# Optimization experiments

Hardware: AMD Instinct MI355X
Metric: run time of the kernel (lower is better)

The kernel has to match this reference:

```python
import jax, jax.numpy as jnp
import numpy as np

H = 5
THETA = 1e-4
RHO = 1e-5


def setup_inputs() -> dict:
    key = jax.random.key(0)
    kw, kb, kv = jax.random.split(key, 3)
    # keras random_normal_initializer(mean=0.5/0.1, stddev=0.05) + NonNeg constraint
    w = jnp.abs(0.5 + 0.05 * jax.random.normal(kw, (1, H), dtype=jnp.float32))
    b = jnp.abs(0.1 + 0.05 * jax.random.normal(kb, (H - 1,), dtype=jnp.float32))
    v = jnp.abs(0.5 + 0.05 * jax.random.normal(kv, (H, 1), dtype=jnp.float32))
    return {"w": w, "b": b, "v": v, "k": 16384}


def _gen_gaps(w, b, v, k):
    dt = jnp.float32
    wf = jnp.reshape(w, (-1,)).astype(dt)            # (H,)
    vf = jnp.reshape(v, (-1,)).astype(dt)            # (H,)
    bf = jnp.concatenate([jnp.zeros((1,), dt), b.astype(dt)])  # (H,), b[0]==0
    v0 = -jnp.dot(bf, vf)                            # scalar, matches -(b @ v)
    c = jnp.asarray(THETA + RHO, dt)
    p = jnp.asarray(THETA / (THETA + RHO), dt)
    K2 = k + 2

    def inverse(x):
        # faithful to source: only breakpoint i=0 is used (for i in range(1))
        b_over_w = -bf / wf
        r_x = jnp.dot(jax.nn.relu(wf * b_over_w[0] + bf), vf) + v0  # scalar
        bounds = jnp.sort(jnp.stack([jnp.asarray(0.0, dt), r_x, jnp.asarray(jnp.inf, dt)]))
        pos = jnp.searchsorted(bounds, x, side='right')
        # argsort of length-1 r_x is [0]; v_b/v_w are length-1 gathers
        v_b0 = vf[0] * bf[0]
        v_w0 = vf[0] * wf[0]
        gate = (pos >= 2).astype(dt)                 # sum over [:pos-1] of length-1 arrays
        num = x - v0 - gate * v_b0
        deo = gate * v_w0
        safe = jnp.where(deo != 0, deo, jnp.asarray(1.0, dt))
        return jnp.where(deo != 0, num / safe, jnp.asarray(0.0, dt))  # divide_no_nan

    key = jax.random.key(1234)
    key, k0 = jax.random.split(key)
    z0 = -jnp.log(jax.random.uniform(k0, (), dtype=dt))
    x0 = inverse(z0)

    max_steps = 2 * K2 + 256  # safe bound: ~1.1*(k+2) steps needed in expectation

    def step(carry, subkey):
        j, pos, x, inner = carry
        u1, u2, u3, u4 = jax.random.uniform(subkey, (4,), dtype=dt)
        active = j < K2
        do_inner = inner & active
        do_outer = jnp.logical_and(~inner, active)
        # --- outer body: u = runif(); z = rexp(); x = inverse(z + r(u*x)) ---
        u_x = u1 * x
        z = -jnp.log(u2)
        r_u_x = v0 + jnp.dot(jax.nn.relu(wf * u_x + bf), vf)
        x_new = inverse(z + r_u_x)
        x2 = jnp.where(do_outer, x_new, x)
        # --- inner write (inner mode records pos BEFORE the increment) ---
        wgate = do_inner.astype(dt)
        val = pos * wgate
        idx = jnp.where(do_inner, j, K2)  # dummy slot K2 when not writing
        j2 = j + do_inner.astype(j.dtype)
        # --- pos += rexp() / (x * (theta + rho)) in both modes ---
        e = -jnp.log(u3)
        pos2 = pos + jnp.where(active, e / (x2 * c), jnp.asarray(0.0, dt))
        # --- inner-loop continuation check: runif() < theta/(theta+rho) and j < k+2 ---
        inner2 = jnp.where(active, (u4 < p) & (j2 < K2), inner)
        return (j2, pos2, x2, inner2), (val, idx)

    keys = jax.random.split(key, max_steps)
    init = (jnp.int32(0), jnp.asarray(0.0, dt), x0, jnp.asarray(False))
    _, (vals, idxs) = jax.lax.scan(step, init, keys)
    ta = jnp.zeros((K2 + 1,), dt).at[idxs].add(vals)[:K2]  # TensorArray of size k+2
    ret = ta[1:]
    diff = ret[1:] - ret[:-1]
    return diff.reshape(1, k)


def reference(w, b, v, k):
    return _gen_gaps(w, b, v, k)
```

## Files before the change

kernel.cpp:

```cpp
#include <hip/hip_runtime.h>
#include <stdint.h>

#define H_MAX 8
#define NT 4096
#define K1T 256
#define K1B (NT / K1T)
#define K2T 1024
#define NW 16

__host__ __device__ __forceinline__ uint32_t rotl32(uint32_t v, int d) {
  return (v << d) | (v >> (32 - d));
}

__host__ __device__ __forceinline__ void tf2x32(uint32_t k0, uint32_t k1,
                                                uint32_t x0, uint32_t x1,
                                                uint32_t& o0, uint32_t& o1) {
  const uint32_t ks2 = k0 ^ k1 ^ 0x1BD11BDAu;
#define TFR(d) { x0 += x1; x1 = rotl32(x1, d); x1 ^= x0; }
  x0 += k0; x1 += k1;
  TFR(13) TFR(15) TFR(26) TFR(6)
  x0 += k1;  x1 += ks2 + 1u;
  TFR(17) TFR(29) TFR(16) TFR(24)
  x0 += ks2; x1 += k0 + 2u;
  TFR(13) TFR(15) TFR(26) TFR(6)
  x0 += k0;  x1 += k1 + 3u;
  TFR(17) TFR(29) TFR(16) TFR(24)
  x0 += k1;  x1 += ks2 + 4u;
  TFR(13) TFR(15) TFR(26) TFR(6)
  x0 += ks2; x1 += k0 + 5u;
#undef TFR
  o0 = x0; o1 = x1;
}

__device__ __forceinline__ float u01f(uint32_t bits) {
  return __uint_as_float((bits >> 9) | 0x3f800000u) - 1.0f;
}

__device__ __forceinline__ uint32_t pbits32(uint32_t k0, uint32_t k1, uint32_t i) {
  uint32_t o0, o1;
  tf2x32(k0, k1, 0u, i, o0, o1);
  return o0 ^ o1;
}

__global__ __launch_bounds__(K1T) void rng_kernel(const float* __restrict__ w,
                                                  const float* __restrict__ bb,
                                                  const float* __restrict__ vv,
                                                  float4* __restrict__ pre,
                                                  float* __restrict__ out,
                                                  int k, int H,
                                                  uint32_t sk0, uint32_t sk1) {
  const int t = blockIdx.x * K1T + threadIdx.x;

  float wf[H_MAX], bf[H_MAX], vf[H_MAX];
  for (int h = 0; h < H; ++h) {
    wf[h] = w[h];
    vf[h] = vv[h];
    bf[h] = (h == 0) ? 0.0f : bb[h - 1];
  }
  float sbv = 0.0f, swv = 0.0f;
  for (int h = 0; h < H; ++h) { sbv += bf[h] * vf[h]; swv += wf[h] * vf[h]; }
  const float ivw  = 1.0f / (vf[0] * wf[0]);
  const float GAIN = swv * ivw;
  const float C_F  = (float)(0.0001 + 1e-05);
  const float RCF  = 1.0f / C_F;

  for (int i4 = t; i4 * 4 + 3 < k; i4 += NT)
    ((float4*)out)[i4] = make_float4(0.0f, 0.0f, 0.0f, 0.0f);

  uint32_t a0, a1;
  tf2x32(sk0, sk1, 0u, (uint32_t)t, a0, a1);
  float u1 = u01f(pbits32(a0, a1, 0u));
  float Z  = -logf(u01f(pbits32(a0, a1, 1u)));
  float E  = -logf(u01f(pbits32(a0, a1, 2u)));
  float u4 = u01f(pbits32(a0, a1, 3u));
  int slot = (t & 3) * K2T + (t >> 2);
  pre[slot] = make_float4(u1 * GAIN, (Z + sbv) * ivw, E * RCF, u4);
}

__global__ __launch_bounds__(K2T, 1) void scan_kernel(const float* __restrict__ w,
                                                      const float* __restrict__ bb,
                                                      const float* __restrict__ vv,
                                                      const float4* __restrict__ pre,
                                                      float* __restrict__ out,
                                                      int k, int K2, int B, int H,
                                                      uint32_t sk0, uint32_t sk1,
                                                      uint32_t z0bits) {
  __shared__ double Aw[NW], Cw[NW];
  __shared__ float  Sw[NW];
  __shared__ int    Fw[NW];
  __shared__ float  sh_u4[K2T];
  __shared__ float  ta[NT];
  __shared__ double finX;
  __shared__ float  finP;
  __shared__ int    jfin;

  const int tid  = threadIdx.x;
  const int lane = tid & 63;
  const int wid  = tid >> 6;

  float wf[H_MAX], bf[H_MAX], vf[H_MAX];
  for (int h = 0; h < H; ++h) {
    wf[h] = w[h];
    vf[h] = vv[h];
    bf[h] = (h == 0) ? 0.0f : bb[h - 1];
  }
  float sbv = 0.0f, swv = 0.0f;
  for (int h = 0; h < H; ++h) { sbv += bf[h] * vf[h]; swv += wf[h] * vf[h]; }
  const float ivw  = 1.0f / (vf[0] * wf[0]);
  const float GAIN = swv * ivw;
  const float C_F  = (float)(0.0001 + 1e-05);
  const float P_F  = (float)(0.0001 / (0.0001 + 1e-05));
  const float RCF  = 1.0f / C_F;
  const float INF  = __builtin_inff();

  float4 r0 = pre[0 * K2T + tid];
  float4 r1 = pre[1 * K2T + tid];
  float4 r2 = pre[2 * K2T + tid];
  float4 r3 = pre[3 * K2T + tid];

  sh_u4[tid] = r3.w;
  __syncthreads();
  float u4m1 = (tid == 0) ? 2.0f : sh_u4[tid - 1];
  bool fl0 = (u4m1 < P_F);
  bool fl1 = (r0.w < P_F);
  bool fl2 = (r1.w < P_F);
  bool fl3 = (r2.w < P_F);
  double a0d = fl0 ? 1.0 : (double)r0.x, c0d = fl0 ? 0.0 : (double)r0.y;
  double a1d = fl1 ? 1.0 : (double)r1.x, c1d = fl1 ? 0.0 : (double)r1.y;
  double a2d = fl2 ? 1.0 : (double)r2.x, c2d = fl2 ? 0.0 : (double)r2.y;
  double a3d = fl3 ? 1.0 : (double)r3.x, c3d = fl3 ? 0.0 : (double)r3.y;

  double A = 1.0, C = 0.0;
  C = a0d * C + c0d;  A = a0d * A;
  C = a1d * C + c1d;  A = a1d * A;
  C = a2d * C + c2d;  A = a2d * A;
  C = a3d * C + c3d;  A = a3d * A;
  for (int d = 1; d < 64; d <<= 1) {
    double Ap = __shfl_up(A, d);
    double Cp = __shfl_up(C, d);
    if (lane >= d) { C = A * Cp + C; A = A * Ap; }
  }
  if (lane == 63) { Aw[wid] = A; Cw[wid] = C; }
  __syncthreads();
  double Awp = 1.0, Cwp = 0.0;
  for (int q = 0; q < wid; ++q) {
    double Aq = Aw[q], Cq = Cw[q];
    Cwp = Aq * Cwp + Cq;
    Awp = Aq * Awp;
  }
  double Aex = __shfl_up(A, 1), Cex = __shfl_up(C, 1);
  if (lane == 0) { Aex = 1.0; Cex = 0.0; }
  double Ag = Aex * Awp;
  double Cg = Aex * Cwp + Cex;

  float z0  = -logf(u01f(z0bits));
  float x0f = (z0 + sbv) * ivw;
  double X = Ag * (double)x0f + Cg;
  float inc0, inc1, inc2, inc3;
  X = a0d * X + c0d;  inc0 = r0.z * __builtin_amdgcn_rcpf((float)X);
  X = a1d * X + c1d;  inc1 = r1.z * __builtin_amdgcn_rcpf((float)X);
  X = a2d * X + c2d;  inc2 = r2.z * __builtin_amdgcn_rcpf((float)X);
  X = a3d * X + c3d;  inc3 = r3.z * __builtin_amdgcn_rcpf((float)X);
  float Sl = inc0 + inc1 + inc2 + inc3;
  int Fl = (fl0 ? 1 : 0) + (fl1 ? 1 : 0) + (fl2 ? 1 : 0) + (fl3 ? 1 : 0);

  float S = Sl; int F = Fl;
  for (int d = 1; d < 64; d <<= 1) {
    float Sp = __shfl_up(S, d);
    int   Fp = __shfl_up(F, d);
    if (lane >= d) { S += Sp; F += Fp; }
  }
  if (lane == 63) { Sw[wid] = S; Fw[wid] = F; }
  __syncthreads();
  float Swp = 0.0f; int Fwp = 0;
  for (int q = 0; q < wid; ++q) { Swp += Sw[q]; Fwp += Fw[q]; }
  float Sex = __shfl_up(S, 1); int Fex = __shfl_up(F, 1);
  if (lane == 0) { Sex = 0.0f; Fex = 0; }
  float P0 = Swp + Sex;
  int   J0 = Fwp + Fex;

  {
    float P = P0; int J = J0;
    if (fl0) { if (J < NT) ta[J] = P; ++J; }  P += inc0;
    if (fl1) { if (J < NT) ta[J] = P; ++J; }  P += inc1;
    if (fl2) { if (J < NT) ta[J] = P; ++J; }  P += inc2;
    if (fl3) { if (J < NT) ta[J] = P; ++J; }  P += inc3;
    if (tid == K2T - 1) { finX = X; finP = P; jfin = J; }
  }
  __syncthreads();

  {
    int J = J0;
    if (fl0) { if (J >= 2 && J < NT && (J - 2) < k) out[J - 2] = ta[J] - ta[J - 1]; ++J; }
    if (fl1) { if (J >= 2 && J < NT && (J - 2) < k) out[J - 2] = ta[J] - ta[J - 1]; ++J; }
    if (fl2) { if (J >= 2 && J < NT && (J - 2) < k) out[J - 2] = ta[J] - ta[J - 1]; ++J; }
    if (fl3) { if (J >= 2 && J < NT && (J - 2) < k) out[J - 2] = ta[J] - ta[J - 1]; ++J; }
  }

  double Xf = finX;
  if (Xf >= 1e30) return;
  if (tid >= 64) return;
  {
    float x = (float)Xf;
    float rcx = __builtin_amdgcn_rcpf(x);
    float pos = finP;
    int j = jfin;
    float pos_prev = (j >= 1 && j <= NT) ? ta[j - 1] : 0.0f;
    bool inner = (sh_u4[K2T - 1] < P_F) && (j < K2);
    bool done = false;
    for (int base = NT; base < B && !done; base += 64) {
      int t = base + lane;
      if (t >= B) t = B - 1;
      uint32_t a0, a1;
      tf2x32(sk0, sk1, 0u, (uint32_t)t, a0, a1);
      float aa = u01f(pbits32(a0, a1, 0u)) * GAIN;
      float cc = (-logf(u01f(pbits32(a0, a1, 1u))) + sbv) * ivw;
      float EE = -logf(u01f(pbits32(a0, a1, 2u))) * RCF;
      float u4 = u01f(pbits32(a0, a1, 3u));
      int lim = (B - base) < 64 ? (B - base) : 64;
      for (int s = 0; s < lim; ++s) {
        float Af = __shfl(aa, s);
        float Cf = __shfl(cc, s);
        float Ef = __shfl(EE, s);
        float U4 = __shfl(u4, s);
        if (inner) {
          if (j >= 2 && (j - 2) < k) out[j - 2] = pos - pos_prev;
          pos_prev = pos; ++j;
        } else {
          x = __builtin_fmaf(Af, x, Cf);
          rcx = __builtin_amdgcn_rcpf(x);
        }
        pos = __builtin_fmaf(Ef, rcx, pos);
        inner = (U4 < P_F) && (j < K2);
        if (x == INF || j >= K2) {
          if (x == INF && j >= 2 && (j - 2) < k) out[j - 2] = pos - pos_prev;
          done = true; break;
        }
      }
    }
    if (!done && j >= 2 && (j - 2) < k) out[j - 2] = 0.0f - pos_prev;
  }
}

extern "C" void kernel_launch(void* const* d_in, const int* in_sizes, int n_in,
                              void* d_out, int out_size, void* d_ws, size_t ws_size,
                              hipStream_t stream) {
  const float* w = (const float*)d_in[0];
  const float* b = (const float*)d_in[1];
  const float* v = (const float*)d_in[2];
  (void)n_in; (void)ws_size;
  const int H  = in_sizes[0];
  const int k  = out_size;
  const int K2 = k + 2;
  const int B  = 2 * K2 + 256;

  uint32_t ka0, ka1, kb0, kb1;
  tf2x32(0u, 1234u, 0u, 0u, ka0, ka1);
  tf2x32(0u, 1234u, 0u, 1u, kb0, kb1);
  uint32_t zb0, zb1;
  tf2x32(kb0, kb1, 0u, 0u, zb0, zb1);
  const uint32_t z0bits = zb0 ^ zb1;

  float4* pre = (float4*)d_ws;

  rng_kernel<<<dim3(K1B), K1T, 0, stream>>>(w, b, v, pre, (float*)d_out,
                                            k, H, ka0, ka1);
  scan_kernel<<<dim3(1), K2T, 0, stream>>>(w, b, v, pre, (float*)d_out,
                                           k, K2, B, H, ka0, ka1, z0bits);
}
```

Baseline: 17.74 us.

## Fuse RNG and scan kernels into one launch with inter-block flag sync

Merges the RNG precompute kernel and the single-block scan kernel into one launch. Block 0 runs the scan and spin-waits on per-block flags in global memory, while 16 producer blocks each generate 256 RNG tuples, zero the output and set a magic flag after a threadfence. The goal is to remove the second kernel launch and the gap between launches. It relies on all 17 blocks being co-resident, adds spin-wait cost, and requires the flags to be reset to zero for the next call, which the scan block does.

```diff
diff --git a/kernel.cpp b/kernel.cpp
--- a/kernel.cpp
+++ b/kernel.cpp
@@ -3,10 +3,11 @@
 
 #define H_MAX 8
 #define NT 4096
-#define K1T 256
-#define K1B (NT / K1T)
 #define K2T 1024
 #define NW 16
+#define NRB 16
+#define RSTEPS 256
+#define MAGIC 0x5EED5EEDu
 
 __host__ __device__ __forceinline__ uint32_t rotl32(uint32_t v, int d) {
   return (v << d) | (v >> (32 - d));
@@ -42,14 +43,16 @@
   return o0 ^ o1;
 }
 
-__global__ __launch_bounds__(K1T) void rng_kernel(const float* __restrict__ w,
-                                                  const float* __restrict__ bb,
-                                                  const float* __restrict__ vv,
-                                                  float4* __restrict__ pre,
-                                                  float* __restrict__ out,
-                                                  int k, int H,
-                                                  uint32_t sk0, uint32_t sk1) {
-  const int t = blockIdx.x * K1T + threadIdx.x;
+__global__ __launch_bounds__(K2T, 1) void gaps_fused(const float* __restrict__ w,
+                                                     const float* __restrict__ bb,
+                                                     const float* __restrict__ vv,
+                                                     float4* __restrict__ pre,
+                                                     uint32_t* __restrict__ flagsv,
+                                                     float* __restrict__ out,
+                                                     int k, int K2, int B, int H,
+                                                     uint32_t sk0, uint32_t sk1,
+                                                     uint32_t z0bits) {
+  const int tid = threadIdx.x;
 
   float wf[H_MAX], bf[H_MAX], vf[H_MAX];
   for (int h = 0; h < H; ++h) {
@@ -62,29 +65,32 @@
   const float ivw  = 1.0f / (vf[0] * wf[0]);
   const float GAIN = swv * ivw;
   const float C_F  = (float)(0.0001 + 1e-05);
+  const float P_F  = (float)(0.0001 / (0.0001 + 1e-05));
   const float RCF  = 1.0f / C_F;
-
-  for (int i4 = t; i4 * 4 + 3 < k; i4 += NT)
-    ((float4*)out)[i4] = make_float4(0.0f, 0.0f, 0.0f, 0.0f);
-
-  uint32_t a0, a1;
-  tf2x32(sk0, sk1, 0u, (uint32_t)t, a0, a1);
-  float u1 = u01f(pbits32(a0, a1, 0u));
-  float Z  = -logf(u01f(pbits32(a0, a1, 1u)));
-  float E  = -logf(u01f(pbits32(a0, a1, 2u)));
-  float u4 = u01f(pbits32(a0, a1, 3u));
-  int slot = (t & 3) * K2T + (t >> 2);
-  pre[slot] = make_float4(u1 * GAIN, (Z + sbv) * ivw, E * RCF, u4);
-}
-
-__global__ __launch_bounds__(K2T, 1) void scan_kernel(const float* __restrict__ w,
-                                                      const float* __restrict__ bb,
-                                                      const float* __restrict__ vv,
-                                                      const float4* __restrict__ pre,
-                                                      float* __restrict__ out,
-                                                      int k, int K2, int B, int H,
-                                                      uint32_t sk0, uint32_t sk1,
-                                                      uint32_t z0bits) {
+  const float INF  = __builtin_inff();
+
+  if (blockIdx.x > 0) {
+    const int b = blockIdx.x - 1;
+    const int gtid = b * K2T + tid;
+    for (int i4 = gtid; i4 * 4 + 3 < k; i4 += NRB * K2T)
+      ((float4*)out)[i4] = make_float4(0.0f, 0.0f, 0.0f, 0.0f);
+    if (tid < RSTEPS) {
+      const int t = b * RSTEPS + tid;
+      uint32_t a0, a1;
+      tf2x32(sk0, sk1, 0u, (uint32_t)t, a0, a1);
+      float u1 = u01f(pbits32(a0, a1, 0u));
+      float Z  = -logf(u01f(pbits32(a0, a1, 1u)));
+      float E  = -logf(u01f(pbits32(a0, a1, 2u)));
+      float u4 = u01f(pbits32(a0, a1, 3u));
+      int slot = (t & 3) * K2T + (t >> 2);
+      pre[slot] = make_float4(u1 * GAIN, (Z + sbv) * ivw, E * RCF, u4);
+    }
+    __threadfence();
+    __syncthreads();
+    if (tid == 0) atomicExch(&flagsv[b], MAGIC);
+    return;
+  }
+
   __shared__ double Aw[NW], Cw[NW];
   __shared__ float  Sw[NW];
   __shared__ int    Fw[NW];
@@ -94,24 +100,17 @@
   __shared__ float  finP;
   __shared__ int    jfin;
 
-  const int tid  = threadIdx.x;
   const int lane = tid & 63;
   const int wid  = tid >> 6;
 
-  float wf[H_MAX], bf[H_MAX], vf[H_MAX];
-  for (int h = 0; h < H; ++h) {
-    wf[h] = w[h];
-    vf[h] = vv[h];
-    bf[h] = (h == 0) ? 0.0f : bb[h - 1];
-  }
-  float sbv = 0.0f, swv = 0.0f;
-  for (int h = 0; h < H; ++h) { sbv += bf[h] * vf[h]; swv += wf[h] * vf[h]; }
-  const float ivw  = 1.0f / (vf[0] * wf[0]);
-  const float GAIN = swv * ivw;
-  const float C_F  = (float)(0.0001 + 1e-05);
-  const float P_F  = (float)(0.0001 / (0.0001 + 1e-05));
-  const float RCF  = 1.0f / C_F;
-  const float INF  = __builtin_inff();
+  float z0  = -logf(u01f(z0bits));
+  float x0f = (z0 + sbv) * ivw;
+
+  if (tid < NRB) {
+    while (atomicAdd(&flagsv[tid], 0u) != MAGIC) __builtin_amdgcn_s_sleep(2);
+    __threadfence();
+  }
+  __syncthreads();
 
   float4 r0 = pre[0 * K2T + tid];
   float4 r1 = pre[1 * K2T + tid];
@@ -120,6 +119,7 @@
 
   sh_u4[tid] = r3.w;
   __syncthreads();
+  if (tid < NRB) atomicExch(&flagsv[tid], 0u);
   float u4m1 = (tid == 0) ? 2.0f : sh_u4[tid - 1];
   bool fl0 = (u4m1 < P_F);
   bool fl1 = (r0.w < P_F);
@@ -153,8 +153,6 @@
   double Ag = Aex * Awp;
   double Cg = Aex * Cwp + Cex;
 
-  float z0  = -logf(u01f(z0bits));
-  float x0f = (z0 + sbv) * ivw;
   double X = Ag * (double)x0f + Cg;
   float inc0, inc1, inc2, inc3;
   X = a0d * X + c0d;  inc0 = r0.z * __builtin_amdgcn_rcpf((float)X);
@@ -261,10 +259,10 @@
   tf2x32(kb0, kb1, 0u, 0u, zb0, zb1);
   const uint32_t z0bits = zb0 ^ zb1;
 
-  float4* pre = (float4*)d_ws;
-
-  rng_kernel<<<dim3(K1B), K1T, 0, stream>>>(w, b, v, pre, (float*)d_out,
-                                            k, H, ka0, ka1);
-  scan_kernel<<<dim3(1), K2T, 0, stream>>>(w, b, v, pre, (float*)d_out,
-                                           k, K2, B, H, ka0, ka1, z0bits);
-}
+  float4*   pre   = (float4*)d_ws;
+  uint32_t* flags = (uint32_t*)((char*)d_ws + NT * 16);
+
+  gaps_fused<<<dim3(NRB + 1), K2T, 0, stream>>>(w, b, v, pre, flags,
+                                                (float*)d_out,
+                                                k, K2, B, H, ka0, ka1, z0bits);
+}
```

Measured after the change: 18.83 us. 1.06x slower.
